# Kernel tuning notes

Measured on AMD Instinct MI355X. Metric: run time of the kernel, lower is better.

The kernel has to match this reference:

```python
import jax, jax.numpy as jnp
import numpy as np

N = 100000       # nodes
E = 1600000      # edges (avg degree 16)
IN_DIM = 64
HID_DIM = 128
OUT_DIM = 64

def setup_inputs() -> dict:
    key = jax.random.key(0)
    k = jax.random.split(key, 8)
    inp = jax.random.normal(k[0], (IN_DIM, N), dtype=jnp.float32)
    src = jax.random.randint(k[1], (E,), 0, N, dtype=jnp.int32)
    dst = jax.random.randint(k[2], (E,), 0, N, dtype=jnp.int32)
    # Linear params (torch nn.Linear: y = x @ W.T + b)
    s1 = 1.0 / np.sqrt(IN_DIM)
    W1 = jax.random.uniform(k[3], (HID_DIM, IN_DIM), jnp.float32, -s1, s1)
    b1 = jax.random.uniform(k[4], (HID_DIM,), jnp.float32, -s1, s1)
    s2 = 1.0 / np.sqrt(HID_DIM)
    W2 = jax.random.uniform(k[5], (OUT_DIM, HID_DIM), jnp.float32, -s2, s2)
    b2 = jax.random.uniform(k[6], (OUT_DIM,), jnp.float32, -s2, s2)
    return {"inp": inp, "src": src, "dst": dst, "W1": W1, "b1": b1, "W2": W2, "b2": b2}

def reference(inp, src, dst, W1, b1, W2, b2):
    # inp: [in_dim, N] (module passes transposed features)
    X = inp.T                                   # [N, in_dim] node features
    # update_all(copy_src, sum): gather src features, scatter-add at dst
    agg = jax.ops.segment_sum(X[src], dst, num_segments=X.shape[0])  # [N, in_dim]
    h = jax.nn.relu(agg @ W1.T + b1)            # [N, hidden]
    out = h @ W2.T + b2                         # [N, out_dim]
    return out.T                                 # [out_dim, N] (final .t())
```

## Files before the change

### kernel.cpp

```cpp
#include <hip/hip_runtime.h>
#include <hip/hip_bf16.h>
#include <stdint.h>

typedef unsigned short ushort_t;
using short8   = __attribute__((ext_vector_type(8))) short;
using float4v  = __attribute__((ext_vector_type(4))) float;
using uint4v   = __attribute__((ext_vector_type(4))) unsigned;

#define BSH    6
#define BUCKW  64
#define CAP    1536
#define NBMAX  2048
#define BINB   384
#define HPITCH 136
#define APITCH 36

__device__ __forceinline__ ushort_t f2b(float f) {
    union { float f; unsigned int i; } v;
    v.f = f;
    unsigned int u = v.i;
    unsigned int r = (u + 0x7fffu + ((u >> 16) & 1u)) >> 16;
    return (ushort_t)r;
}
__device__ __forceinline__ float blo2f(unsigned v) {
    union { unsigned i; float f; } u; u.i = v << 16; return u.f;
}
__device__ __forceinline__ float bhi2f(unsigned v) {
    union { unsigned i; float f; } u; u.i = v & 0xFFFF0000u; return u.f;
}

__global__ __launch_bounds__(512) void prep_k(
        const float* __restrict__ inp, ushort_t* __restrict__ X, int N,
        const float* __restrict__ W1, const float* __restrict__ W2,
        ushort_t* __restrict__ w1b, ushort_t* __restrict__ w2b,
        const int* __restrict__ src, const int* __restrict__ dst,
        int* __restrict__ gcur, unsigned* __restrict__ bin, int E,
        int NB) {
    __shared__ int lcnt[NBMAX];
    __shared__ int gbase[NBMAX];
    __shared__ int lcur[NBMAX];
    int tid = threadIdx.x;

    if ((int)blockIdx.x >= BINB) {
        int tb = blockIdx.x - BINB;
        if (tb == 0) {
            for (int i = tid; i < 8192; i += 512) {
                w1b[i] = f2b(W1[i]);
                w2b[i] = f2b(W2[i]);
            }
        }
        int db = tid >> 7;
        int nl = tid & 127;
        int nc = tb * 128 + nl;
        if (nc < N) {
            const float* ip = inp + (size_t)(db * 16) * N + nc;
            float v[16];
#pragma unroll
            for (int r = 0; r < 16; ++r)
                v[r] = ip[(size_t)r * N];
            unsigned dw[8];
#pragma unroll
            for (int j = 0; j < 8; ++j)
                dw[j] = (unsigned)f2b(v[2 * j]) | ((unsigned)f2b(v[2 * j + 1]) << 16);
            unsigned* xp = (unsigned*)X + (size_t)nc * 32 + db * 8;
            uint4v a = {dw[0], dw[1], dw[2], dw[3]};
            uint4v b = {dw[4], dw[5], dw[6], dw[7]};
            *(uint4v*)(xp)     = a;
            *(uint4v*)(xp + 4) = b;
        }
    } else {
        int bid   = blockIdx.x;
        int chunk = (E + BINB - 1) / BINB;
        int s0 = bid * chunk;
        int s1 = s0 + chunk;
        if (s1 > E) s1 = E;

        for (int b = tid; b < NB; b += 512) lcnt[b] = 0;
        __syncthreads();

        int e = s0 + tid;
        for (; e + 512 * 7 < s1; e += 512 * 8) {
            int d[8];
#pragma unroll
            for (int k = 0; k < 8; ++k) d[k] = dst[e + 512 * k];
#pragma unroll
            for (int k = 0; k < 8; ++k) atomicAdd(&lcnt[d[k] >> BSH], 1);
        }
        for (; e < s1; e += 512)
            atomicAdd(&lcnt[dst[e] >> BSH], 1);
        __syncthreads();

        for (int b = tid; b < NB; b += 512) {
            int c = lcnt[b];
            gbase[b] = c ? atomicAdd(&gcur[b], c) : 0;
            lcur[b]  = 0;
        }
        __syncthreads();

        e = s0 + tid;
        for (; e + 512 * 7 < s1; e += 512 * 8) {
            int d[8], s[8];
#pragma unroll
            for (int k = 0; k < 8; ++k) {
                d[k] = dst[e + 512 * k];
                s[k] = src[e + 512 * k];
            }
#pragma unroll
            for (int k = 0; k < 8; ++k) {
                int b   = d[k] >> BSH;
                int pos = gbase[b] + atomicAdd(&lcur[b], 1);
                if (pos < CAP)
                    bin[(size_t)b * CAP + pos] =
                        ((unsigned)(d[k] & (BUCKW - 1)) << 24) | (unsigned)s[k];
            }
        }
        for (; e < s1; e += 512) {
            int dv = dst[e];
            int b  = dv >> BSH;
            int pos = gbase[b] + atomicAdd(&lcur[b], 1);
            if (pos < CAP)
                bin[(size_t)b * CAP + pos] =
                    ((unsigned)(dv & (BUCKW - 1)) << 24) | (unsigned)src[e];
        }
    }
}

__global__ __launch_bounds__(256, 6) void bam_k(
        const unsigned* __restrict__ Xu, const unsigned* __restrict__ bin,
        const int* __restrict__ gcur,
        const ushort_t* __restrict__ W1, const float* __restrict__ b1,
        const ushort_t* __restrict__ W2, const float* __restrict__ b2,
        float* __restrict__ out, int N) {
    __shared__ unsigned agg_s[BUCKW * APITCH];
    __shared__ __align__(16) char pool[4 * 16 * HPITCH * 2];
    unsigned* sl  = (unsigned*)pool;
    int* ecnt = (int*)(pool + CAP * 4);
    int* sc   = ecnt + BUCKW;
    int* ecur = sc + BUCKW;

    int tid = threadIdx.x;
    int b   = blockIdx.x;

    int cnt = gcur[b];
    if (cnt > CAP) cnt = CAP;
    const unsigned* bb = bin + (size_t)b * CAP;

    if (tid < BUCKW) ecnt[tid] = 0;
    __syncthreads();

    for (int i = tid; i < cnt; i += 256)
        atomicAdd(&ecnt[bb[i] >> 24], 1);
    __syncthreads();

    if (tid < BUCKW) sc[tid] = ecnt[tid];
    __syncthreads();
#pragma unroll
    for (int off = 1; off < BUCKW; off <<= 1) {
        int v = 0;
        if (tid < BUCKW && tid >= off) v = sc[tid - off];
        __syncthreads();
        if (tid < BUCKW) sc[tid] += v;
        __syncthreads();
    }
    if (tid < BUCKW) { sc[tid] -= ecnt[tid]; ecur[tid] = 0; }
    __syncthreads();

    for (int i = tid; i < cnt; i += 256) {
        unsigned p = bb[i];
        int nl  = (int)(p >> 24);
        int pos = sc[nl] + atomicAdd(&ecur[nl], 1);
        sl[pos] = p;
    }
    __syncthreads();

    int wave = tid >> 6;
    int lane = tid & 63;
    int half = lane >> 5;
    unsigned cu = (unsigned)(lane & 31);
    int row  = lane & 15;
    int quad = lane >> 4;

    for (int n = wave; n < BUCKW; n += 4) {
        int s0 = sc[n];
        int c  = ecnt[n];
        float alo0 = 0.f, ahi0 = 0.f, alo1 = 0.f, ahi1 = 0.f;
        int i = 0;
        for (; i + 16 <= c; i += 16) {
            unsigned p0 = sl[s0 + i +  0 + half], p1 = sl[s0 + i +  2 + half];
            unsigned p2 = sl[s0 + i +  4 + half], p3 = sl[s0 + i +  6 + half];
            unsigned p4 = sl[s0 + i +  8 + half], p5 = sl[s0 + i + 10 + half];
            unsigned p6 = sl[s0 + i + 12 + half], p7 = sl[s0 + i + 14 + half];
            unsigned v0 = Xu[((p0 & 0xFFFFFFu) << 5) | cu];
            unsigned v1 = Xu[((p1 & 0xFFFFFFu) << 5) | cu];
            unsigned v2 = Xu[((p2 & 0xFFFFFFu) << 5) | cu];
            unsigned v3 = Xu[((p3 & 0xFFFFFFu) << 5) | cu];
            unsigned v4 = Xu[((p4 & 0xFFFFFFu) << 5) | cu];
            unsigned v5 = Xu[((p5 & 0xFFFFFFu) << 5) | cu];
            unsigned v6 = Xu[((p6 & 0xFFFFFFu) << 5) | cu];
            unsigned v7 = Xu[((p7 & 0xFFFFFFu) << 5) | cu];
            alo0 += blo2f(v0); ahi0 += bhi2f(v0);
            alo1 += blo2f(v1); ahi1 += bhi2f(v1);
            alo0 += blo2f(v2); ahi0 += bhi2f(v2);
            alo1 += blo2f(v3); ahi1 += bhi2f(v3);
            alo0 += blo2f(v4); ahi0 += bhi2f(v4);
            alo1 += blo2f(v5); ahi1 += bhi2f(v5);
            alo0 += blo2f(v6); ahi0 += bhi2f(v6);
            alo1 += blo2f(v7); ahi1 += bhi2f(v7);
        }
        for (; i + 2 <= c; i += 2) {
            unsigned p = sl[s0 + i + half];
            unsigned v = Xu[((p & 0xFFFFFFu) << 5) | cu];
            alo0 += blo2f(v); ahi0 += bhi2f(v);
        }
        if (i + half < c) {
            unsigned p = sl[s0 + i + half];
            unsigned v = Xu[((p & 0xFFFFFFu) << 5) | cu];
            alo1 += blo2f(v); ahi1 += bhi2f(v);
        }
        float alo = alo0 + alo1;
        float ahi = ahi0 + ahi1;
        float blo = __shfl(alo, lane + 32);
        float bhi = __shfl(ahi, lane + 32);
        if (half == 0) {
            alo += blo; ahi += bhi;
            agg_s[n * APITCH + (int)cu] =
                (unsigned)f2b(alo) | ((unsigned)f2b(ahi) << 16);
        }
    }
    __syncthreads();

    ushort_t* hw = (ushort_t*)pool + (size_t)wave * (16 * HPITCH);

    const unsigned* arow = agg_s + (wave * 16 + row) * APITCH;
    short8 a0 = *(const short8*)(arow + quad * 4);
    short8 a1 = *(const short8*)(arow + 16 + quad * 4);

    float4v zero = {0.f, 0.f, 0.f, 0.f};

#pragma unroll
    for (int g = 0; g < 2; ++g) {
        float4v acc[4];
#pragma unroll
        for (int nt = 0; nt < 4; ++nt) acc[nt] = zero;
#pragma unroll
        for (int nt = 0; nt < 4; ++nt) {
            const ushort_t* wp = W1 + (size_t)(g * 64 + nt * 16 + row) * 64 + quad * 8;
            short8 bf0 = *(const short8*)(wp);
            short8 bf1 = *(const short8*)(wp + 32);
            acc[nt] = __builtin_amdgcn_mfma_f32_16x16x32_bf16(a0, bf0, acc[nt], 0, 0, 0);
            acc[nt] = __builtin_amdgcn_mfma_f32_16x16x32_bf16(a1, bf1, acc[nt], 0, 0, 0);
        }
#pragma unroll
        for (int nt = 0; nt < 4; ++nt) {
            float bias = b1[g * 64 + nt * 16 + row];
#pragma unroll
            for (int r = 0; r < 4; ++r) {
                float v = acc[nt][r] + bias;
                v = v > 0.f ? v : 0.f;
                hw[(quad * 4 + r) * HPITCH + g * 64 + nt * 16 + row] = f2b(v);
            }
        }
    }
    __syncthreads();

    short8 a2[4];
#pragma unroll
    for (int kt = 0; kt < 4; ++kt)
        a2[kt] = *(const short8*)(hw + row * HPITCH + kt * 32 + quad * 8);

    float4v acc2[4];
#pragma unroll
    for (int nt = 0; nt < 4; ++nt) acc2[nt] = zero;

#pragma unroll
    for (int nt = 0; nt < 4; ++nt) {
#pragma unroll
        for (int kt = 0; kt < 4; ++kt) {
            short8 bfr = *(const short8*)(W2 + (size_t)(nt * 16 + row) * 128 +
                                          kt * 32 + quad * 8);
            acc2[nt] = __builtin_amdgcn_mfma_f32_16x16x32_bf16(a2[kt], bfr, acc2[nt], 0, 0, 0);
        }
    }

    int n0   = (b << BSH) + wave * 16;
    int node = n0 + quad * 4;
#pragma unroll
    for (int nt = 0; nt < 4; ++nt) {
        int ko = nt * 16 + row;
        float bias = b2[ko];
        float4v pk;
#pragma unroll
        for (int r = 0; r < 4; ++r) pk[r] = acc2[nt][r] + bias;
        if (node + 3 < N) {
            *(float4v*)(out + (size_t)ko * N + node) = pk;
        } else {
#pragma unroll
            for (int r = 0; r < 4; ++r)
                if (node + r < N) out[(size_t)ko * N + node + r] = pk[r];
        }
    }
}

__global__ __launch_bounds__(256) void bagg_k(
        const unsigned* __restrict__ Xu, const unsigned* __restrict__ bin,
        const int* __restrict__ gcur, unsigned* __restrict__ aggu, int N) {
    __shared__ unsigned sl[CAP];
    __shared__ int ecnt[BUCKW];
    __shared__ int sc[BUCKW];
    __shared__ int ecur[BUCKW];
    int tid = threadIdx.x;
    int b   = blockIdx.x;
    int lo  = b << BSH;

    int cnt = gcur[b];
    if (cnt > CAP) cnt = CAP;
    const unsigned* bb = bin + (size_t)b * CAP;

    if (tid < BUCKW) ecnt[tid] = 0;
    __syncthreads();
    for (int i = tid; i < cnt; i += 256)
        atomicAdd(&ecnt[bb[i] >> 24], 1);
    __syncthreads();
    if (tid < BUCKW) sc[tid] = ecnt[tid];
    __syncthreads();
#pragma unroll
    for (int off = 1; off < BUCKW; off <<= 1) {
        int v = 0;
        if (tid < BUCKW && tid >= off) v = sc[tid - off];
        __syncthreads();
        if (tid < BUCKW) sc[tid] += v;
        __syncthreads();
    }
    if (tid < BUCKW) { sc[tid] -= ecnt[tid]; ecur[tid] = 0; }
    __syncthreads();
    for (int i = tid; i < cnt; i += 256) {
        unsigned p = bb[i];
        int nl  = (int)(p >> 24);
        int pos = sc[nl] + atomicAdd(&ecur[nl], 1);
        sl[pos] = p;
    }
    __syncthreads();

    int wave = tid >> 6;
    int lane = tid & 63;
    int half = lane >> 5;
    unsigned cu = (unsigned)(lane & 31);

    for (int n = wave; n < BUCKW; n += 4) {
        int node = lo + n;
        if (node >= N) break;
        int s0 = sc[n];
        int c  = ecnt[n];
        float alo0 = 0.f, ahi0 = 0.f, alo1 = 0.f, ahi1 = 0.f;
        int i = 0;
        for (; i + 16 <= c; i += 16) {
            unsigned p0 = sl[s0 + i +  0 + half], p1 = sl[s0 + i +  2 + half];
            unsigned p2 = sl[s0 + i +  4 + half], p3 = sl[s0 + i +  6 + half];
            unsigned p4 = sl[s0 + i +  8 + half], p5 = sl[s0 + i + 10 + half];
            unsigned p6 = sl[s0 + i + 12 + half], p7 = sl[s0 + i + 14 + half];
            unsigned v0 = Xu[((p0 & 0xFFFFFFu) << 5) | cu];
            unsigned v1 = Xu[((p1 & 0xFFFFFFu) << 5) | cu];
            unsigned v2 = Xu[((p2 & 0xFFFFFFu) << 5) | cu];
            unsigned v3 = Xu[((p3 & 0xFFFFFFu) << 5) | cu];
            unsigned v4 = Xu[((p4 & 0xFFFFFFu) << 5) | cu];
            unsigned v5 = Xu[((p5 & 0xFFFFFFu) << 5) | cu];
            unsigned v6 = Xu[((p6 & 0xFFFFFFu) << 5) | cu];
            unsigned v7 = Xu[((p7 & 0xFFFFFFu) << 5) | cu];
            alo0 += blo2f(v0); ahi0 += bhi2f(v0);
            alo1 += blo2f(v1); ahi1 += bhi2f(v1);
            alo0 += blo2f(v2); ahi0 += bhi2f(v2);
            alo1 += blo2f(v3); ahi1 += bhi2f(v3);
            alo0 += blo2f(v4); ahi0 += bhi2f(v4);
            alo1 += blo2f(v5); ahi1 += bhi2f(v5);
            alo0 += blo2f(v6); ahi0 += bhi2f(v6);
            alo1 += blo2f(v7); ahi1 += bhi2f(v7);
        }
        for (; i + 2 <= c; i += 2) {
            unsigned p = sl[s0 + i + half];
            unsigned v = Xu[((p & 0xFFFFFFu) << 5) | cu];
            alo0 += blo2f(v); ahi0 += bhi2f(v);
        }
        if (i + half < c) {
            unsigned p = sl[s0 + i + half];
            unsigned v = Xu[((p & 0xFFFFFFu) << 5) | cu];
            alo1 += blo2f(v); ahi1 += bhi2f(v);
        }
        float alo = alo0 + alo1;
        float ahi = ahi0 + ahi1;
        float blo = __shfl(alo, lane + 32);
        float bhi = __shfl(ahi, lane + 32);
        if (half == 0) {
            alo += blo; ahi += bhi;
            aggu[(size_t)node * 32 + (int)cu] =
                (unsigned)f2b(alo) | ((unsigned)f2b(ahi) << 16);
        }
    }
}

__global__ __launch_bounds__(256) void mlp_k(
        const ushort_t* __restrict__ aggb,
        const ushort_t* __restrict__ W1, const float* __restrict__ b1,
        const ushort_t* __restrict__ W2, const float* __restrict__ b2,
        float* __restrict__ out, int N) {
    __shared__ ushort_t h_s[4][16 * HPITCH];

    int wave = threadIdx.x >> 6;
    int lane = threadIdx.x & 63;
    int row  = lane & 15;
    int quad = lane >> 4;
    int n0   = blockIdx.x * 64 + wave * 16;

    int anode = n0 + row;
    if (anode > N - 1) anode = N - 1;
    const ushort_t* ap = aggb + (size_t)anode * 64;
    short8 a0 = *(const short8*)(ap + quad * 8);
    short8 a1 = *(const short8*)(ap + 32 + quad * 8);

    float4v zero = {0.f, 0.f, 0.f, 0.f};
    float4v acc[8];
#pragma unroll
    for (int nt = 0; nt < 8; ++nt) acc[nt] = zero;

#pragma unroll
    for (int nt = 0; nt < 8; ++nt) {
        const ushort_t* wp = W1 + (size_t)(nt * 16 + row) * 64 + quad * 8;
        short8 bf0 = *(const short8*)(wp);
        short8 bf1 = *(const short8*)(wp + 32);
        acc[nt] = __builtin_amdgcn_mfma_f32_16x16x32_bf16(a0, bf0, acc[nt], 0, 0, 0);
        acc[nt] = __builtin_amdgcn_mfma_f32_16x16x32_bf16(a1, bf1, acc[nt], 0, 0, 0);
    }

    ushort_t* hw = h_s[wave];
#pragma unroll
    for (int nt = 0; nt < 8; ++nt) {
        float bias = b1[nt * 16 + row];
#pragma unroll
        for (int r = 0; r < 4; ++r) {
            float v = acc[nt][r] + bias;
            v = v > 0.f ? v : 0.f;
            hw[(quad * 4 + r) * HPITCH + nt * 16 + row] = f2b(v);
        }
    }
    __syncthreads();

    short8 a2[4];
#pragma unroll
    for (int kt = 0; kt < 4; ++kt)
        a2[kt] = *(const short8*)(hw + row * HPITCH + kt * 32 + quad * 8);

    float4v acc2[4];
#pragma unroll
    for (int nt = 0; nt < 4; ++nt) acc2[nt] = zero;

#pragma unroll
    for (int nt = 0; nt < 4; ++nt) {
#pragma unroll
        for (int kt = 0; kt < 4; ++kt) {
            short8 bfr = *(const short8*)(W2 + (size_t)(nt * 16 + row) * 128 +
                                          kt * 32 + quad * 8);
            acc2[nt] = __builtin_amdgcn_mfma_f32_16x16x32_bf16(a2[kt], bfr, acc2[nt], 0, 0, 0);
        }
    }

    int node = n0 + quad * 4;
    if (node < N) {
#pragma unroll
        for (int nt = 0; nt < 4; ++nt) {
            int ko = nt * 16 + row;
            float bias = b2[ko];
            float4v pk;
#pragma unroll
            for (int r = 0; r < 4; ++r) pk[r] = acc2[nt][r] + bias;
            *(float4v*)(out + (size_t)ko * N + node) = pk;
        }
    }
}

extern "C" void kernel_launch(void* const* d_in, const int* in_sizes, int n_in,
                              void* d_out, int out_size, void* d_ws, size_t ws_size,
                              hipStream_t stream) {
    const float* inp = (const float*)d_in[0];
    const int*   src = (const int*)d_in[1];
    const int*   dst = (const int*)d_in[2];
    const float* W1  = (const float*)d_in[3];
    const float* b1  = (const float*)d_in[4];
    const float* W2  = (const float*)d_in[5];
    const float* b2  = (const float*)d_in[6];
    float* out = (float*)d_out;

    int N  = in_sizes[0] / 64;
    int E  = in_sizes[1];
    int NB = (N + BUCKW - 1) >> BSH;
    int TB = (N + 127) / 128;

    size_t xBytes    = (size_t)N * 64 * 2;
    size_t binBytes  = (size_t)NB * CAP * 4;
    size_t fusedNeed = xBytes + binBytes + 2 * 8192 * 2 + NBMAX * 4 + 64;

    if (ws_size >= fusedNeed) {
        char* w = (char*)d_ws;
        ushort_t* X    = (ushort_t*)w;
        unsigned* bin  = (unsigned*)(w + xBytes);
        ushort_t* w1b  = (ushort_t*)(w + xBytes + binBytes);
        ushort_t* w2b  = w1b + 8192;
        int*      gcur = (int*)(w2b + 8192);

        hipMemsetAsync(gcur, 0, NB * sizeof(int), stream);

        prep_k<<<BINB + TB, 512, 0, stream>>>(inp, X, N, W1, W2, w1b, w2b,
                                              src, dst, gcur, bin, E, NB);

        bam_k<<<NB, 256, 0, stream>>>((const unsigned*)X, bin, gcur,
                                      w1b, b1, w2b, b2, out, N);
    } else {
        ushort_t* aggb = (ushort_t*)d_ws;
        ushort_t* w1b  = aggb + (size_t)N * 64;
        ushort_t* w2b  = w1b + 8192;
        int*      gcur = (int*)(w2b + 8192);

        char*     ob  = (char*)d_out;
        ushort_t* X   = (ushort_t*)ob;
        unsigned* bin = (unsigned*)(ob + xBytes);

        hipMemsetAsync(gcur, 0, NB * sizeof(int), stream);

        prep_k<<<BINB + TB, 512, 0, stream>>>(inp, X, N, W1, W2, w1b, w2b,
                                              src, dst, gcur, bin, E, NB);

        bagg_k<<<NB, 256, 0, stream>>>((const unsigned*)X, bin, gcur,
                                       (unsigned*)aggb, N);

        int tb = (N + 63) / 64;
        mlp_k<<<tb, 256, 0, stream>>>(aggb, w1b, b1, w2b, b2, out, N);
    }
}
```

Measured before the change: 214.7 us.

## Double fused aggregate+MLP block to 512 threads and split MLP across waves

Raises the fused gather/MLP kernel from 256 to 512 threads per block. Eight waves now share the per-node gather loop, and the MLP work is split so each wave handles half of the hidden columns and half of the output columns. The shared-memory buffers are overlaid into a single 17 KB pool, and the block-level prefix scan is replaced with a wave-level shuffle scan that drops several barriers. This adds parallelism per bucket and cuts synchronisation, but it adds an extra barrier and lowers the requested blocks per CU.

```diff
diff --git a/kernel.cpp b/kernel.cpp
--- a/kernel.cpp
+++ b/kernel.cpp
@@ -125,18 +125,18 @@
     }
 }
 
-__global__ __launch_bounds__(256, 6) void bam_k(
+__global__ __launch_bounds__(512, 3) void bam_k(
         const unsigned* __restrict__ Xu, const unsigned* __restrict__ bin,
         const int* __restrict__ gcur,
         const ushort_t* __restrict__ W1, const float* __restrict__ b1,
         const ushort_t* __restrict__ W2, const float* __restrict__ b2,
         float* __restrict__ out, int N) {
-    __shared__ unsigned agg_s[BUCKW * APITCH];
-    __shared__ __align__(16) char pool[4 * 16 * HPITCH * 2];
-    unsigned* sl  = (unsigned*)pool;
-    int* ecnt = (int*)(pool + CAP * 4);
-    int* sc   = ecnt + BUCKW;
-    int* ecur = sc + BUCKW;
+    __shared__ __align__(16) char P[17408];
+    unsigned* sl    = (unsigned*)P;
+    int*      ecnt  = (int*)(P + 6144);
+    int*      sc    = (int*)(P + 6400);
+    int*      ecur  = (int*)(P + 6656);
+    unsigned* agg_s = (unsigned*)(P + 6912);
 
     int tid = threadIdx.x;
     int b   = blockIdx.x;
@@ -148,24 +148,23 @@
     if (tid < BUCKW) ecnt[tid] = 0;
     __syncthreads();
 
-    for (int i = tid; i < cnt; i += 256)
+    for (int i = tid; i < cnt; i += 512)
         atomicAdd(&ecnt[bb[i] >> 24], 1);
     __syncthreads();
 
-    if (tid < BUCKW) sc[tid] = ecnt[tid];
-    __syncthreads();
-#pragma unroll
-    for (int off = 1; off < BUCKW; off <<= 1) {
-        int v = 0;
-        if (tid < BUCKW && tid >= off) v = sc[tid - off];
-        __syncthreads();
-        if (tid < BUCKW) sc[tid] += v;
-        __syncthreads();
-    }
-    if (tid < BUCKW) { sc[tid] -= ecnt[tid]; ecur[tid] = 0; }
-    __syncthreads();
-
-    for (int i = tid; i < cnt; i += 256) {
+    if (tid < BUCKW) {
+        int v = ecnt[tid];
+#pragma unroll
+        for (int off = 1; off < BUCKW; off <<= 1) {
+            int t = __shfl_up(v, off, 64);
+            if (tid >= off) v += t;
+        }
+        sc[tid]   = v - ecnt[tid];
+        ecur[tid] = 0;
+    }
+    __syncthreads();
+
+    for (int i = tid; i < cnt; i += 512) {
         unsigned p = bb[i];
         int nl  = (int)(p >> 24);
         int pos = sc[nl] + atomicAdd(&ecur[nl], 1);
@@ -180,7 +179,7 @@
     int row  = lane & 15;
     int quad = lane >> 4;
 
-    for (int n = wave; n < BUCKW; n += 4) {
+    for (int n = wave; n < BUCKW; n += 8) {
         int s0 = sc[n];
         int c  = ecnt[n];
         float alo0 = 0.f, ahi0 = 0.f, alo1 = 0.f, ahi1 = 0.f;
@@ -229,22 +228,25 @@
     }
     __syncthreads();
 
-    ushort_t* hw = (ushort_t*)pool + (size_t)wave * (16 * HPITCH);
-
-    const unsigned* arow = agg_s + (wave * 16 + row) * APITCH;
+    int grp    = wave & 3;
+    int g_half = wave >> 2;
+
+    const unsigned* arow = agg_s + (grp * 16 + row) * APITCH;
     short8 a0 = *(const short8*)(arow + quad * 4);
     short8 a1 = *(const short8*)(arow + 16 + quad * 4);
 
+    __syncthreads();
+
+    ushort_t* hw = (ushort_t*)P + (size_t)grp * (16 * HPITCH);
     float4v zero = {0.f, 0.f, 0.f, 0.f};
 
-#pragma unroll
-    for (int g = 0; g < 2; ++g) {
+    {
         float4v acc[4];
 #pragma unroll
         for (int nt = 0; nt < 4; ++nt) acc[nt] = zero;
 #pragma unroll
         for (int nt = 0; nt < 4; ++nt) {
-            const ushort_t* wp = W1 + (size_t)(g * 64 + nt * 16 + row) * 64 + quad * 8;
+            const ushort_t* wp = W1 + (size_t)(g_half * 64 + nt * 16 + row) * 64 + quad * 8;
             short8 bf0 = *(const short8*)(wp);
             short8 bf1 = *(const short8*)(wp + 32);
             acc[nt] = __builtin_amdgcn_mfma_f32_16x16x32_bf16(a0, bf0, acc[nt], 0, 0, 0);
@@ -252,12 +254,12 @@
         }
 #pragma unroll
         for (int nt = 0; nt < 4; ++nt) {
-            float bias = b1[g * 64 + nt * 16 + row];
+            float bias = b1[g_half * 64 + nt * 16 + row];
 #pragma unroll
             for (int r = 0; r < 4; ++r) {
                 float v = acc[nt][r] + bias;
                 v = v > 0.f ? v : 0.f;
-                hw[(quad * 4 + r) * HPITCH + g * 64 + nt * 16 + row] = f2b(v);
+                hw[(quad * 4 + r) * HPITCH + g_half * 64 + nt * 16 + row] = f2b(v);
             }
         }
     }
@@ -268,25 +270,26 @@
     for (int kt = 0; kt < 4; ++kt)
         a2[kt] = *(const short8*)(hw + row * HPITCH + kt * 32 + quad * 8);
 
-    float4v acc2[4];
-#pragma unroll
-    for (int nt = 0; nt < 4; ++nt) acc2[nt] = zero;
-
-#pragma unroll
-    for (int nt = 0; nt < 4; ++nt) {
+    float4v acc2[2];
+#pragma unroll
+    for (int nt = 0; nt < 2; ++nt) acc2[nt] = zero;
+
+#pragma unroll
+    for (int nt = 0; nt < 2; ++nt) {
+        int ntg = g_half * 2 + nt;
 #pragma unroll
         for (int kt = 0; kt < 4; ++kt) {
-            short8 bfr = *(const short8*)(W2 + (size_t)(nt * 16 + row) * 128 +
+            short8 bfr = *(const short8*)(W2 + (size_t)(ntg * 16 + row) * 128 +
                                           kt * 32 + quad * 8);
             acc2[nt] = __builtin_amdgcn_mfma_f32_16x16x32_bf16(a2[kt], bfr, acc2[nt], 0, 0, 0);
         }
     }
 
-    int n0   = (b << BSH) + wave * 16;
+    int n0   = (b << BSH) + grp * 16;
     int node = n0 + quad * 4;
 #pragma unroll
-    for (int nt = 0; nt < 4; ++nt) {
-        int ko = nt * 16 + row;
+    for (int nt = 0; nt < 2; ++nt) {
+        int ko = (g_half * 2 + nt) * 16 + row;
         float bias = b2[ko];
         float4v pk;
 #pragma unroll
@@ -510,7 +513,7 @@
         prep_k<<<BINB + TB, 512, 0, stream>>>(inp, X, N, W1, W2, w1b, w2b,
                                               src, dst, gcur, bin, E, NB);
 
-        bam_k<<<NB, 256, 0, stream>>>((const unsigned*)X, bin, gcur,
+        bam_k<<<NB, 512, 0, stream>>>((const unsigned*)X, bin, gcur,
                                       w1b, b1, w2b, b2, out, N);
     } else {
         ushort_t* aggb = (ushort_t*)d_ws;
```

Result: faster. 190.4 us (-11.3%).
